# Optimization experiments

Measured on AMD Instinct MI355X. Metric: run time of the kernel, lower is better.

## Reference

```python
import jax, jax.numpy as jnp
import numpy as np

B, S, D, H = 32, 2048, 256, 256  # batch, seq_len, input_size, hidden_size


def setup_inputs() -> dict:
    key = jax.random.key(0)
    ks = jax.random.split(key, 9)
    s = 0.05  # small init scale to keep gates in a sane range
    return {
        "inputs": jax.random.normal(ks[0], (B, S, D), dtype=jnp.float32),
        "W_ih0": jax.random.normal(ks[1], (3 * H, D), dtype=jnp.float32) * s,
        "W_hh0": jax.random.normal(ks[2], (3 * H, H), dtype=jnp.float32) * s,
        "b_ih0": jax.random.normal(ks[3], (3 * H,), dtype=jnp.float32) * s,
        "b_hh0": jax.random.normal(ks[4], (3 * H,), dtype=jnp.float32) * s,
        "W_ih1": jax.random.normal(ks[5], (3 * H, 2 * H), dtype=jnp.float32) * s,
        "W_hh1": jax.random.normal(ks[6], (3 * H, H), dtype=jnp.float32) * s,
        "b_ih1": jax.random.normal(ks[7], (3 * H,), dtype=jnp.float32) * s,
        "b_hh1": jax.random.normal(ks[8], (3 * H,), dtype=jnp.float32) * s,
    }


def _gru_scan(gx, W_hh, b_hh, reverse):
    """gx: [S,B,3H] precomputed input projections. Returns ([S,B,H] states in
    original time order, [B,H] final carry). lax.scan(reverse=True) stores
    outputs at matching time positions, which matches the module's flip(1)."""
    Hh = W_hh.shape[1]
    h0 = jnp.zeros((gx.shape[1], Hh), gx.dtype)

    def step(h, gx_t):
        gh = h @ W_hh.T + b_hh                      # [B,3H]
        xr, xz, xn = jnp.split(gx_t, 3, axis=-1)
        hr, hz, hn = jnp.split(gh, 3, axis=-1)
        r = jax.nn.sigmoid(xr + hr)
        z = jax.nn.sigmoid(xz + hz)
        n = jnp.tanh(xn + r * hn)
        h_new = (1.0 - z) * n + z * h               # torch.nn.GRUCell update
        return h_new, h_new

    h_last, hs = jax.lax.scan(step, h0, gx, reverse=reverse)
    return hs, h_last


def _bidir_layer(x, W_ih, W_hh, b_ih, b_hh):
    # Precompute all input-to-hidden GEMMs in one batched matmul.
    gx = jnp.einsum('bsd,gd->sbg', x, W_ih) + b_ih  # [S,B,3H]
    # cells_backward is a deepcopy of cells_forward -> identical weights.
    hs_f, hf = _gru_scan(gx, W_hh, b_hh, reverse=False)
    hs_b, hb = _gru_scan(gx, W_hh, b_hh, reverse=True)
    out = jnp.concatenate([hs_f, hs_b], axis=-1).transpose(1, 0, 2)  # [B,S,2H]
    return out, hf, hb


def reference(inputs, W_ih0, W_hh0, b_ih0, b_hh0, W_ih1, W_hh1, b_ih1, b_hh1):
    out0, hf0, hb0 = _bidir_layer(inputs, W_ih0, W_hh0, b_ih0, b_hh0)
    out1, hf1, hb1 = _bidir_layer(out0, W_ih1, W_hh1, b_ih1, b_hh1)
    # h_n order: (layer0 fwd, layer0 bwd, layer1 fwd, layer1 bwd)
    h_n = jnp.stack([hf0, hb0, hf1, hb1])           # [layers*dirs, B, H]
    return out1, h_n
```

## Files before the change

### kernel.cpp

```cpp
#include <hip/hip_runtime.h>

typedef __attribute__((ext_vector_type(4))) float f32x4;
typedef __attribute__((ext_vector_type(8))) short bf16x8;
typedef __attribute__((ext_vector_type(4))) _Float16 f16x4;

constexpr int kB = 32;
constexpr int kS = 2048;
constexpr int kH = 256;
constexpr int kG = 768;

__device__ __forceinline__ short f2bf(float f) {
  unsigned u = __builtin_bit_cast(unsigned, f);
  u += 0x7fffu + ((u >> 16) & 1u);
  return (short)(u >> 16);
}

__device__ __forceinline__ float fast_sigmoid(float x) {
  return __builtin_amdgcn_rcpf(1.0f + __builtin_amdgcn_exp2f(x * -1.4426950408889634f));
}
__device__ __forceinline__ float fast_tanh(float x) {
  float e = __builtin_amdgcn_exp2f(x * 2.8853900817779268f);
  return 1.0f - 2.0f * __builtin_amdgcn_rcpf(1.0f + e);
}

__device__ __forceinline__ void load8(const float* p, float v[8]) {
  const float4 a = *(const float4*)p;
  const float4 b = *(const float4*)(p + 4);
  v[0] = a.x; v[1] = a.y; v[2] = a.z; v[3] = a.w;
  v[4] = b.x; v[5] = b.y; v[6] = b.z; v[7] = b.w;
}

template <int LAYER>
__global__ __launch_bounds__(256) void gemm_gx(
    const void* __restrict__ Av, const float* __restrict__ W,
    const float* __restrict__ b_ih, const float* __restrict__ b_hh,
    _Float16* __restrict__ gx) {
  constexpr int K = (LAYER == 0) ? 256 : 512;
  __shared__ short As[64][40];
  __shared__ short Ws[64][40];
  const int tid = threadIdx.x;
  const int lane = tid & 63, wv = tid >> 6;
  const int quad = lane >> 4, l15 = lane & 15;
  const int m0 = blockIdx.y * 64, n0 = blockIdx.x * 64;
  const int srow = tid >> 2, kq = tid & 3;
  const int am = m0 + srow;
  const int b = am & 31, s = am >> 5;
  const float* Wrow = W + (size_t)(n0 + srow) * K;
  const float* Af = (const float*)Av + ((size_t)b * kS + s) * 256;
  const short* Ab = (const short*)Av + ((size_t)s * 64 + b) * 256;

  f32x4 acc[4] = {};

  for (int k0 = 0; k0 < K; k0 += 32) {
    const int k = k0 + kq * 8;
    short avs[8];
    if constexpr (LAYER == 0) {
      float v[8];
      load8(Af + k, v);
#pragma unroll
      for (int j = 0; j < 8; ++j) avs[j] = f2bf(v[j]);
    } else {
      *(uint4*)avs = *(const uint4*)(Ab + (size_t)(k >> 8) * 8192 + (k & 255));
    }
    float wv8[8];
    load8(Wrow + k, wv8);
    __syncthreads();
#pragma unroll
    for (int j = 0; j < 8; ++j) As[srow][kq * 8 + j] = avs[j];
#pragma unroll
    for (int j = 0; j < 8; ++j) Ws[srow][kq * 8 + j] = f2bf(wv8[j]);
    __syncthreads();
    const bf16x8 bf = *(const bf16x8*)&Ws[wv * 16 + l15][quad * 8];
#pragma unroll
    for (int mt = 0; mt < 4; ++mt) {
      const bf16x8 af = *(const bf16x8*)&As[mt * 16 + l15][quad * 8];
      acc[mt] = __builtin_amdgcn_mfma_f32_16x16x32_bf16(af, bf, acc[mt], 0, 0, 0);
    }
  }
  const int col = n0 + wv * 16 + l15;
  const float bias = b_ih[col] + (col < 512 ? b_hh[col] : 0.0f);
#pragma unroll
  for (int mt = 0; mt < 4; ++mt) {
#pragma unroll
    for (int r = 0; r < 4; ++r) {
      const int m = m0 + mt * 16 + quad * 4 + r;
      gx[((size_t)(m >> 5) * kG + col) * 32 + (m & 31)] = (_Float16)(acc[mt][r] + bias);
    }
  }
}

union Frag8 {
  bf16x8 v;
  uint2 u2[2];
};

template <int LAYER>
__global__ __launch_bounds__(512, 2) void gru_scan(
    const _Float16* __restrict__ gx,
    const float* __restrict__ W_hh,
    const float* __restrict__ b_hh,
    void* __restrict__ outv,
    float* __restrict__ hn) {
  __shared__ short hlds[2][16][264];
  __shared__ short wlds[768][36];

  const int tid = threadIdx.x;
  const int lane = tid & 63;
  const int w = tid >> 6;
  const int quad = lane >> 4, l15 = lane & 15;
  const int dir = blockIdx.x & 1;
  const int bbase = (blockIdx.x >> 1) * 16;

  for (int i = tid; i < 2 * 16 * 264; i += 512) (&hlds[0][0][0])[i] = 0;

  {
    const int kq = tid & 3, rb = tid >> 2;
#pragma unroll
    for (int j = 0; j < 6; ++j) {
      const int row = rb + j * 128;
      float v[8];
      load8(W_hh + (size_t)row * kH + 224 + kq * 8, v);
#pragma unroll
      for (int e = 0; e < 8; ++e) wlds[row][kq * 8 + e] = f2bf(v[e]);
    }
  }

  const int colH0 = w * 32 + l15;
  bf16x8 Bf[3][2][7];
#pragma unroll
  for (int g3 = 0; g3 < 3; ++g3)
#pragma unroll
    for (int nt = 0; nt < 2; ++nt)
#pragma unroll
      for (int kb = 0; kb < 7; ++kb) {
        const int row = g3 * 256 + colH0 + nt * 16;
        float v[8];
        load8(W_hh + (size_t)row * kH + kb * 32 + quad * 8, v);
        bf16x8 f;
#pragma unroll
        for (int e = 0; e < 8; ++e) f[e] = f2bf(v[e]);
        Bf[g3][nt][kb] = f;
      }

  const float bhn[2] = {b_hh[512 + colH0], b_hh[512 + colH0 + 16]};
  float hprev[8] = {0, 0, 0, 0, 0, 0, 0, 0};

  short* out0 = (short*)outv;
  float* out1 = (float*)outv;

  __syncthreads();

  for (int i = 0; i < kS; ++i) {
    const int t = dir ? (kS - 1 - i) : i;
    const _Float16* gxt = gx + (size_t)t * (kG * 32);
    const short(*hbuf)[264] = hlds[i & 1];
    short(*hnext)[264] = hlds[(i & 1) ^ 1];

    f16x4 gxv[3][2];
#pragma unroll
    for (int g3 = 0; g3 < 3; ++g3)
#pragma unroll
      for (int nt = 0; nt < 2; ++nt)
        gxv[g3][nt] = *(const f16x4*)(gxt + (size_t)(g3 * 256 + colH0 + nt * 16) * 32 +
                                      bbase + quad * 4);

    bf16x8 af[8];
#pragma unroll
    for (int kb = 0; kb < 8; ++kb)
      af[kb] = *(const bf16x8*)&hbuf[l15][kb * 32 + quad * 8];

    f32x4 C0[2] = {}, C1[2] = {}, C2[2] = {};

#define CHAIN(G3, CC)                                                              \
  {                                                                                \
    _Pragma("unroll") for (int kb = 0; kb < 7; ++kb) {                             \
      _Pragma("unroll") for (int nt = 0; nt < 2; ++nt) CC[nt] =                    \
          __builtin_amdgcn_mfma_f32_16x16x32_bf16(af[kb], Bf[G3][nt][kb], CC[nt], 0, 0, 0); \
    }                                                                              \
    _Pragma("unroll") for (int nt = 0; nt < 2; ++nt) {                             \
      Frag8 bf;                                                                    \
      const int row = G3 * 256 + colH0 + nt * 16;                                  \
      bf.u2[0] = *(const uint2*)&wlds[row][quad * 8];                              \
      bf.u2[1] = *(const uint2*)&wlds[row][quad * 8 + 4];                          \
      CC[nt] = __builtin_amdgcn_mfma_f32_16x16x32_bf16(af[7], bf.v, CC[nt], 0, 0, 0); \
    }                                                                              \
  }

    CHAIN(0, C0)
    CHAIN(2, C2)

    float rr[2][4];
#pragma unroll
    for (int nt = 0; nt < 2; ++nt)
#pragma unroll
      for (int r = 0; r < 4; ++r)
        rr[nt][r] = fast_sigmoid((float)gxv[0][nt][r] + C0[nt][r]);

    CHAIN(1, C1)

    float nn[2][4];
#pragma unroll
    for (int nt = 0; nt < 2; ++nt)
#pragma unroll
      for (int r = 0; r < 4; ++r)
        nn[nt][r] = fast_tanh((float)gxv[2][nt][r] + rr[nt][r] * (C2[nt][r] + bhn[nt]));

#pragma unroll
    for (int nt = 0; nt < 2; ++nt) {
#pragma unroll
      for (int r = 0; r < 4; ++r) {
        const float zz = fast_sigmoid((float)gxv[1][nt][r] + C1[nt][r]);
        const int e = nt * 4 + r;
        const float h = nn[nt][r] + zz * (hprev[e] - nn[nt][r]);
        hprev[e] = h;
        hnext[quad * 4 + r][colH0 + nt * 16] = f2bf(h);
        if constexpr (LAYER == 1) {
          out1[((size_t)(bbase + quad * 4 + r) * kS + t) * 512 + dir * 256 + colH0 +
               nt * 16] = h;
        }
      }
    }

    __syncthreads();

    if constexpr (LAYER == 0) {
      const int srow = tid >> 5, schunk = tid & 31;
      *(uint4*)(out0 + (((size_t)t * 2 + dir) * 32 + bbase + srow) * 256 + schunk * 8) =
          *(const uint4*)&hnext[srow][schunk * 8];
    }
  }
#undef CHAIN

#pragma unroll
  for (int nt = 0; nt < 2; ++nt)
#pragma unroll
    for (int r = 0; r < 4; ++r)
      hn[(size_t)(dir * kB + bbase + quad * 4 + r) * kH + colH0 + nt * 16] =
          hprev[nt * 4 + r];
}

extern "C" void kernel_launch(void* const* d_in, const int* in_sizes, int n_in,
                              void* d_out, int out_size, void* d_ws, size_t ws_size,
                              hipStream_t stream) {
  const float* x     = (const float*)d_in[0];
  const float* W_ih0 = (const float*)d_in[1];
  const float* W_hh0 = (const float*)d_in[2];
  const float* b_ih0 = (const float*)d_in[3];
  const float* b_hh0 = (const float*)d_in[4];
  const float* W_ih1 = (const float*)d_in[5];
  const float* W_hh1 = (const float*)d_in[6];
  const float* b_ih1 = (const float*)d_in[7];
  const float* b_hh1 = (const float*)d_in[8];

  float* out1 = (float*)d_out;
  float* hn = out1 + (size_t)kB * kS * 512;

  _Float16* gxb = (_Float16*)d_ws;
  short* out0 = (short*)((char*)d_ws + (size_t)kS * kB * kG * 2);

  dim3 ggrid(kG / 64, (kS * kB) / 64);

  gemm_gx<0><<<ggrid, 256, 0, stream>>>(x, W_ih0, b_ih0, b_hh0, gxb);
  gru_scan<0><<<dim3(4), 512, 0, stream>>>(gxb, W_hh0, b_hh0, out0, hn);
  gemm_gx<1><<<ggrid, 256, 0, stream>>>(out0, W_ih1, b_ih1, b_hh1, gxb);
  gru_scan<1><<<dim3(4), 512, 0, stream>>>(gxb, W_hh1, b_hh1, out1, hn + 2 * kB * kH);
}
```

Before: 7.592 ms.

## Double scan block width to 16 waves, one 16-column tile per wave

The recurrent scan kernel now runs 1024 threads per block instead of 512. Each wave owns one 16-column tile per gate rather than two, which halves each wave's serial MFMA chain per time step. The W_hh slice kept in registers shrinks to 6 k-blocks, the last two k-blocks move to LDS, and the MFMAs are reordered to interleave the three gates with a sched_barrier splitting the step into two phases. The trade-off is more waves joining each per-step __syncthreads, extra LDS reads for the weight fragments, and a tighter register budget per thread.

```diff
diff --git a/kernel.cpp b/kernel.cpp
--- a/kernel.cpp
+++ b/kernel.cpp
@@ -95,14 +95,14 @@
 };
 
 template <int LAYER>
-__global__ __launch_bounds__(512, 2) void gru_scan(
+__global__ __launch_bounds__(1024) void gru_scan(
     const _Float16* __restrict__ gx,
     const float* __restrict__ W_hh,
     const float* __restrict__ b_hh,
     void* __restrict__ outv,
     float* __restrict__ hn) {
   __shared__ short hlds[2][16][264];
-  __shared__ short wlds[768][36];
+  __shared__ short wlds[2][768][36];
 
   const int tid = threadIdx.x;
   const int lane = tid & 63;
@@ -111,39 +111,40 @@
   const int dir = blockIdx.x & 1;
   const int bbase = (blockIdx.x >> 1) * 16;
 
-  for (int i = tid; i < 2 * 16 * 264; i += 512) (&hlds[0][0][0])[i] = 0;
+  for (int i = tid; i < 2 * 16 * 264; i += 1024) (&hlds[0][0][0])[i] = 0;
 
   {
     const int kq = tid & 3, rb = tid >> 2;
 #pragma unroll
-    for (int j = 0; j < 6; ++j) {
-      const int row = rb + j * 128;
+    for (int j = 0; j < 3; ++j) {
+      const int row = rb + j * 256;
+#pragma unroll
+      for (int s = 0; s < 2; ++s) {
+        float v[8];
+        load8(W_hh + (size_t)row * kH + 192 + s * 32 + kq * 8, v);
+#pragma unroll
+        for (int e = 0; e < 8; ++e) wlds[s][row][kq * 8 + e] = f2bf(v[e]);
+      }
+    }
+  }
+
+  const int col = w * 16 + l15;
+  bf16x8 Bf[3][6];
+#pragma unroll
+  for (int g3 = 0; g3 < 3; ++g3)
+#pragma unroll
+    for (int kb = 0; kb < 6; ++kb) {
+      const int row = g3 * 256 + col;
       float v[8];
-      load8(W_hh + (size_t)row * kH + 224 + kq * 8, v);
-#pragma unroll
-      for (int e = 0; e < 8; ++e) wlds[row][kq * 8 + e] = f2bf(v[e]);
-    }
-  }
-
-  const int colH0 = w * 32 + l15;
-  bf16x8 Bf[3][2][7];
-#pragma unroll
-  for (int g3 = 0; g3 < 3; ++g3)
-#pragma unroll
-    for (int nt = 0; nt < 2; ++nt)
-#pragma unroll
-      for (int kb = 0; kb < 7; ++kb) {
-        const int row = g3 * 256 + colH0 + nt * 16;
-        float v[8];
-        load8(W_hh + (size_t)row * kH + kb * 32 + quad * 8, v);
-        bf16x8 f;
-#pragma unroll
-        for (int e = 0; e < 8; ++e) f[e] = f2bf(v[e]);
-        Bf[g3][nt][kb] = f;
-      }
-
-  const float bhn[2] = {b_hh[512 + colH0], b_hh[512 + colH0 + 16]};
-  float hprev[8] = {0, 0, 0, 0, 0, 0, 0, 0};
+      load8(W_hh + (size_t)row * kH + kb * 32 + quad * 8, v);
+      bf16x8 f;
+#pragma unroll
+      for (int e = 0; e < 8; ++e) f[e] = f2bf(v[e]);
+      Bf[g3][kb] = f;
+    }
+
+  const float bhn = b_hh[512 + col];
+  float hprev[4] = {0, 0, 0, 0};
 
   short* out0 = (short*)outv;
   float* out1 = (float*)outv;
@@ -156,87 +157,75 @@
     const short(*hbuf)[264] = hlds[i & 1];
     short(*hnext)[264] = hlds[(i & 1) ^ 1];
 
-    f16x4 gxv[3][2];
+    f16x4 gxv[3];
 #pragma unroll
     for (int g3 = 0; g3 < 3; ++g3)
-#pragma unroll
-      for (int nt = 0; nt < 2; ++nt)
-        gxv[g3][nt] = *(const f16x4*)(gxt + (size_t)(g3 * 256 + colH0 + nt * 16) * 32 +
-                                      bbase + quad * 4);
-
-    bf16x8 af[8];
-#pragma unroll
-    for (int kb = 0; kb < 8; ++kb)
-      af[kb] = *(const bf16x8*)&hbuf[l15][kb * 32 + quad * 8];
-
-    f32x4 C0[2] = {}, C1[2] = {}, C2[2] = {};
-
-#define CHAIN(G3, CC)                                                              \
-  {                                                                                \
-    _Pragma("unroll") for (int kb = 0; kb < 7; ++kb) {                             \
-      _Pragma("unroll") for (int nt = 0; nt < 2; ++nt) CC[nt] =                    \
-          __builtin_amdgcn_mfma_f32_16x16x32_bf16(af[kb], Bf[G3][nt][kb], CC[nt], 0, 0, 0); \
-    }                                                                              \
-    _Pragma("unroll") for (int nt = 0; nt < 2; ++nt) {                             \
-      Frag8 bf;                                                                    \
-      const int row = G3 * 256 + colH0 + nt * 16;                                  \
-      bf.u2[0] = *(const uint2*)&wlds[row][quad * 8];                              \
-      bf.u2[1] = *(const uint2*)&wlds[row][quad * 8 + 4];                          \
-      CC[nt] = __builtin_amdgcn_mfma_f32_16x16x32_bf16(af[7], bf.v, CC[nt], 0, 0, 0); \
-    }                                                                              \
-  }
-
-    CHAIN(0, C0)
-    CHAIN(2, C2)
-
-    float rr[2][4];
-#pragma unroll
-    for (int nt = 0; nt < 2; ++nt)
-#pragma unroll
-      for (int r = 0; r < 4; ++r)
-        rr[nt][r] = fast_sigmoid((float)gxv[0][nt][r] + C0[nt][r]);
-
-    CHAIN(1, C1)
-
-    float nn[2][4];
-#pragma unroll
-    for (int nt = 0; nt < 2; ++nt)
-#pragma unroll
-      for (int r = 0; r < 4; ++r)
-        nn[nt][r] = fast_tanh((float)gxv[2][nt][r] + rr[nt][r] * (C2[nt][r] + bhn[nt]));
-
-#pragma unroll
-    for (int nt = 0; nt < 2; ++nt) {
-#pragma unroll
-      for (int r = 0; r < 4; ++r) {
-        const float zz = fast_sigmoid((float)gxv[1][nt][r] + C1[nt][r]);
-        const int e = nt * 4 + r;
-        const float h = nn[nt][r] + zz * (hprev[e] - nn[nt][r]);
-        hprev[e] = h;
-        hnext[quad * 4 + r][colH0 + nt * 16] = f2bf(h);
-        if constexpr (LAYER == 1) {
-          out1[((size_t)(bbase + quad * 4 + r) * kS + t) * 512 + dir * 256 + colH0 +
-               nt * 16] = h;
+      gxv[g3] = *(const f16x4*)(gxt + (size_t)(g3 * 256 + col) * 32 + bbase + quad * 4);
+
+    f32x4 C[3] = {};
+
+    {
+      bf16x8 af[4];
+#pragma unroll
+      for (int kb = 0; kb < 4; ++kb)
+        af[kb] = *(const bf16x8*)&hbuf[l15][kb * 32 + quad * 8];
+#pragma unroll
+      for (int kb = 0; kb < 4; ++kb)
+#pragma unroll
+        for (int g3 = 0; g3 < 3; ++g3)
+          C[g3] = __builtin_amdgcn_mfma_f32_16x16x32_bf16(af[kb], Bf[g3][kb], C[g3], 0, 0, 0);
+    }
+    __builtin_amdgcn_sched_barrier(0);
+    {
+      bf16x8 af[4];
+#pragma unroll
+      for (int k2 = 0; k2 < 4; ++k2)
+        af[k2] = *(const bf16x8*)&hbuf[l15][(4 + k2) * 32 + quad * 8];
+#pragma unroll
+      for (int k2 = 0; k2 < 2; ++k2)
+#pragma unroll
+        for (int g3 = 0; g3 < 3; ++g3)
+          C[g3] = __builtin_amdgcn_mfma_f32_16x16x32_bf16(af[k2], Bf[g3][4 + k2], C[g3], 0, 0, 0);
+#pragma unroll
+      for (int s = 0; s < 2; ++s)
+#pragma unroll
+        for (int g3 = 0; g3 < 3; ++g3) {
+          Frag8 bf;
+          bf.u2[0] = *(const uint2*)&wlds[s][g3 * 256 + col][quad * 8];
+          bf.u2[1] = *(const uint2*)&wlds[s][g3 * 256 + col][quad * 8 + 4];
+          C[g3] = __builtin_amdgcn_mfma_f32_16x16x32_bf16(af[2 + s], bf.v, C[g3], 0, 0, 0);
         }
+    }
+
+    float rr[4], nn[4];
+#pragma unroll
+    for (int r = 0; r < 4; ++r) rr[r] = fast_sigmoid((float)gxv[0][r] + C[0][r]);
+#pragma unroll
+    for (int r = 0; r < 4; ++r)
+      nn[r] = fast_tanh((float)gxv[2][r] + rr[r] * (C[2][r] + bhn));
+#pragma unroll
+    for (int r = 0; r < 4; ++r) {
+      const float zz = fast_sigmoid((float)gxv[1][r] + C[1][r]);
+      const float h = nn[r] + zz * (hprev[r] - nn[r]);
+      hprev[r] = h;
+      hnext[quad * 4 + r][col] = f2bf(h);
+      if constexpr (LAYER == 1) {
+        out1[((size_t)(bbase + quad * 4 + r) * kS + t) * 512 + dir * 256 + col] = h;
       }
     }
 
     __syncthreads();
 
     if constexpr (LAYER == 0) {
-      const int srow = tid >> 5, schunk = tid & 31;
-      *(uint4*)(out0 + (((size_t)t * 2 + dir) * 32 + bbase + srow) * 256 + schunk * 8) =
-          *(const uint4*)&hnext[srow][schunk * 8];
-    }
-  }
-#undef CHAIN
-
-#pragma unroll
-  for (int nt = 0; nt < 2; ++nt)
-#pragma unroll
-    for (int r = 0; r < 4; ++r)
-      hn[(size_t)(dir * kB + bbase + quad * 4 + r) * kH + colH0 + nt * 16] =
-          hprev[nt * 4 + r];
+      const int srow = tid >> 6, schunk = tid & 63;
+      *(uint2*)(out0 + (((size_t)t * 2 + dir) * 32 + bbase + srow) * 256 + schunk * 4) =
+          *(const uint2*)&hnext[srow][schunk * 4];
+    }
+  }
+
+#pragma unroll
+  for (int r = 0; r < 4; ++r)
+    hn[(size_t)(dir * kB + bbase + quad * 4 + r) * kH + col] = hprev[r];
 }
 
 extern "C" void kernel_launch(void* const* d_in, const int* in_sizes, int n_in,
@@ -261,7 +250,7 @@
   dim3 ggrid(kG / 64, (kS * kB) / 64);
 
   gemm_gx<0><<<ggrid, 256, 0, stream>>>(x, W_ih0, b_ih0, b_hh0, gxb);
-  gru_scan<0><<<dim3(4), 512, 0, stream>>>(gxb, W_hh0, b_hh0, out0, hn);
+  gru_scan<0><<<dim3(4), 1024, 0, stream>>>(gxb, W_hh0, b_hh0, out0, hn);
   gemm_gx<1><<<ggrid, 256, 0, stream>>>(out0, W_ih1, b_ih1, b_hh1, gxb);
-  gru_scan<1><<<dim3(4), 512, 0, stream>>>(gxb, W_hh1, b_hh1, out1, hn + 2 * kB * kH);
-}
+  gru_scan<1><<<dim3(4), 1024, 0, stream>>>(gxb, W_hh1, b_hh1, out1, hn + 2 * kB * kH);
+}
```

Result: faster. 6.704 ms (-11.7%).
